# Performance work log

Hardware: AMD Instinct MI355X
Metric: run time of the kernel (lower is better)

Reference implementation:

```python
import jax, jax.numpy as jnp
import numpy as np
import math

D_MODEL = 64
D_STATE = 16
V_RANGE = 1
K = 3
BATCH, H, W = 4, 32, 32
V_LIST = [(x, y) for x in range(-V_RANGE, V_RANGE + 1) for y in range(-V_RANGE, V_RANGE + 1)]
NUM_V = len(V_LIST)


def _circ_conv(x, w):
    # x: (B, Cin, H, W), w: (Cout, Cin, K, K); circular padding then VALID conv
    p = K // 2
    xp = jnp.pad(x, ((0, 0), (0, 0), (p, p), (p, p)), mode='wrap')
    return jax.lax.conv_general_dilated(
        xp, w, window_strides=(1, 1), padding='VALID',
        dimension_numbers=('NCHW', 'OIHW', 'NCHW'))


def setup_inputs() -> dict:
    key = jax.random.key(0)
    ks = jax.random.split(key, 8)
    fan = 1.0 / math.sqrt(D_MODEL * K * K)
    u_t = jax.random.normal(ks[0], (BATCH, D_MODEL, H, W), dtype=jnp.float32)
    s_prev = jax.random.normal(ks[1], (BATCH, NUM_V, D_MODEL, D_STATE, H, W), dtype=jnp.float32)
    conv_delta_w = jax.random.normal(ks[2], (D_MODEL, D_MODEL, K, K), dtype=jnp.float32) * fan
    conv_delta_b = jax.random.normal(ks[3], (D_MODEL,), dtype=jnp.float32) * 0.01
    conv_B_w = jax.random.normal(ks[4], (D_STATE, D_MODEL, K, K), dtype=jnp.float32) * fan
    conv_C_w = jax.random.normal(ks[5], (D_STATE, D_MODEL, K, K), dtype=jnp.float32) * fan
    log_A_real = jnp.log(0.5 * jnp.ones((D_MODEL, D_STATE), dtype=jnp.float32))
    D = jnp.ones((D_MODEL,), dtype=jnp.float32)
    dt_inv_softplus = jnp.asarray(math.log(math.e - 1.0), dtype=jnp.float32)
    return {
        'u_t': u_t, 's_prev': s_prev,
        'conv_delta_w': conv_delta_w, 'conv_delta_b': conv_delta_b,
        'conv_B_w': conv_B_w, 'conv_C_w': conv_C_w,
        'log_A_real': log_A_real, 'D': D, 'dt_inv_softplus': dt_inv_softplus,
    }


def reference(u_t, s_prev, conv_delta_w, conv_delta_b, conv_B_w, conv_C_w,
              log_A_real, D, dt_inv_softplus):
    # delta: (B, d_model, h, w)
    delta = jax.nn.softplus(_circ_conv(u_t, conv_delta_w)
                            + conv_delta_b[None, :, None, None] + dt_inv_softplus)
    B_val = _circ_conv(u_t, conv_B_w)   # (B, d_state, h, w)
    C_val = _circ_conv(u_t, conv_C_w)   # (B, d_state, h, w)
    A = -jnp.exp(log_A_real)            # (d_model, d_state)
    A_bc = A[None, :, :, None, None]    # (1, d_model, d_state, 1, 1)
    A_bar = jnp.exp(delta[:, :, None] * A_bc)        # (B, d_model, d_state, h, w)
    B_bar = (A_bar - 1.0) / A_bc * B_val[:, None]    # (B, d_model, d_state, h, w)
    u_bc = u_t[:, :, None]              # (B, d_model, 1, h, w)
    C_bc = C_val[:, None]               # (B, 1, d_state, h, w)
    y_skip = u_t * D[None, :, None, None]

    s_next_list, y_list = [], []
    for i, (vx, vy) in enumerate(V_LIST):
        s_tr = jnp.roll(s_prev[:, i], shift=(-vy, -vx), axis=(-2, -1))
        s_new = A_bar * s_tr + B_bar * u_bc          # (B, d_model, d_state, h, w)
        y_new = jnp.sum(s_new * C_bc, axis=2) + y_skip
        s_next_list.append(s_new)
        y_list.append(y_new)
    s_next = jnp.stack(s_next_list, axis=1)  # (B, num_v, d_model, d_state, h, w)
    y_out = jnp.stack(y_list, axis=1)        # (B, num_v, d_model, h, w)
    return (y_out, s_next)
```

## Files before the change

### kernel.cpp

```cpp
#include <hip/hip_runtime.h>
#include <math.h>

#define NBATCH 4
#define NV 9
#define DM 64
#define DS 16

__global__ __launch_bounds__(256) void conv_kernel(
    const float* __restrict__ u, const float* __restrict__ wd,
    const float* __restrict__ bd, const float* __restrict__ wb,
    const float* __restrict__ wc, const float* __restrict__ dtp,
    float* __restrict__ delta_out, float* __restrict__ Bv_out,
    float* __restrict__ Cv_out)
{
    int bx = blockIdx.x;
    int ht = bx & 3;
    int co = (bx >> 2) % 96;
    int b  = bx / (4 * 96);
    int tid = threadIdx.x;
    int h = ht * 8 + (tid >> 5);
    int w = tid & 31;

    const float* wbase = (co < 64) ? (wd + (size_t)co * 576)
                       : (co < 80) ? (wb + (size_t)(co - 64) * 576)
                                   : (wc + (size_t)(co - 80) * 576);

    int wm = (w + 31) & 31, wp = (w + 1) & 31;
    int hm = (h + 31) & 31, hp = (h + 1) & 31;
    const float* ub = u + (size_t)b * 64 * 1024;

    float acc = 0.f;
    #pragma unroll 4
    for (int ci = 0; ci < 64; ++ci) {
        const float* up = ub + ci * 1024;
        const float* r0 = up + hm * 32;
        const float* r1 = up + h * 32;
        const float* r2 = up + hp * 32;
        const float* wq = wbase + ci * 9;
        acc += wq[0] * r0[wm] + wq[1] * r0[w] + wq[2] * r0[wp]
             + wq[3] * r1[wm] + wq[4] * r1[w] + wq[5] * r1[wp]
             + wq[6] * r2[wm] + wq[7] * r2[w] + wq[8] * r2[wp];
    }

    int pix = h * 32 + w;
    if (co < 64) {
        float x = acc + bd[co] + dtp[0];
        float d = (x > 20.f) ? x : log1pf(__expf(x));
        delta_out[((size_t)b * 64 + co) * 1024 + pix] = d;
    } else if (co < 80) {
        Bv_out[((size_t)b * 16 + (co - 64)) * 1024 + pix] = acc;
    } else {
        Cv_out[((size_t)b * 16 + (co - 80)) * 1024 + pix] = acc;
    }
}

__global__ __launch_bounds__(256) void scan_kernel(
    const float* __restrict__ u, const float* __restrict__ s_prev,
    const float* __restrict__ logA, const float* __restrict__ Dp,
    const float* __restrict__ delta_in, const float* __restrict__ Bv,
    const float* __restrict__ Cv,
    float* __restrict__ y_out, float* __restrict__ s_next)
{
    int bx = blockIdx.x;
    int t  = bx & 3;
    int c  = (bx >> 2) & 63;
    int bi = bx >> 8;
    int i  = bi % 9;
    int b  = bi / 9;

    int tid = threadIdx.x;
    int pix = t * 256 + tid;
    int h = pix >> 5, w = pix & 31;

    int vx = i / 3 - 1;
    int vy = i % 3 - 1;
    int hh = (h + vy + 32) & 31;
    int ww = (w + vx + 32) & 31;

    float uv = u[(((size_t)b * 64 + c) << 10) + pix];
    float dv = delta_in[(((size_t)b * 64 + c) << 10) + pix];
    float y  = uv * Dp[c];

    size_t chan = ((size_t)bi * 64 + c) * 16;
    const float* sp  = s_prev + (chan << 10) + hh * 32 + ww;
    float*       sn  = s_next + (chan << 10) + pix;
    const float* bvp = Bv + (((size_t)b * 16) << 10) + pix;
    const float* cvp = Cv + (((size_t)b * 16) << 10) + pix;
    const float* la  = logA + c * 16;

    #pragma unroll
    for (int n = 0; n < 16; ++n) {
        float A    = -__expf(la[n]);
        float ab   = __expf(dv * A);
        float coef = (ab - 1.0f) * __builtin_amdgcn_rcpf(A);
        float bu   = coef * bvp[(size_t)n << 10] * uv;
        float s    = sp[(size_t)n << 10];
        float v    = fmaf(ab, s, bu);
        sn[(size_t)n << 10] = v;
        y = fmaf(v, cvp[(size_t)n << 10], y);
    }
    y_out[((size_t)bi * 64 + c) * 1024 + pix] = y;
}

extern "C" void kernel_launch(void* const* d_in, const int* in_sizes, int n_in,
                              void* d_out, int out_size, void* d_ws, size_t ws_size,
                              hipStream_t stream) {
    const float* u      = (const float*)d_in[0];
    const float* s_prev = (const float*)d_in[1];
    const float* wd     = (const float*)d_in[2];
    const float* bd     = (const float*)d_in[3];
    const float* wb     = (const float*)d_in[4];
    const float* wc     = (const float*)d_in[5];
    const float* logA   = (const float*)d_in[6];
    const float* Dp     = (const float*)d_in[7];
    const float* dtp    = (const float*)d_in[8];

    float* ws    = (float*)d_ws;
    float* delta = ws;
    float* Bv    = ws + 262144;
    float* Cv    = ws + 327680;

    float* y_out  = (float*)d_out;
    float* s_next = y_out + (size_t)NBATCH * NV * DM * 1024;

    conv_kernel<<<dim3(4 * 96 * 4), dim3(256), 0, stream>>>(
        u, wd, bd, wb, wc, dtp, delta, Bv, Cv);
    scan_kernel<<<dim3(4 * 9 * 64 * 4), dim3(256), 0, stream>>>(
        u, s_prev, logA, Dp, delta, Bv, Cv, y_out, s_next);
}
```

Baseline: 120.8 us.

## Vectorize conv and scan kernels to four pixels per thread with float4

Both kernels now process four adjacent pixels per thread. The conv kernel uses float4 row loads plus halo scalars and float4 stores, with four accumulators that reuse loaded inputs across outputs. The scan kernel uses float4 loads and stores for state, B, C and y, and handles the horizontal roll with a lane shuffle inside groups of 8 lanes. Grid sizes shrink 4x, which lowers parallelism for the conv kernel (384 blocks) and raises per-thread register use.

```diff
diff --git a/kernel.cpp b/kernel.cpp
--- a/kernel.cpp
+++ b/kernel.cpp
@@ -5,6 +5,10 @@
 #define NV 9
 #define DM 64
 #define DS 16
+
+__device__ __forceinline__ float softplus_f(float x) {
+    return (x > 20.f) ? x : log1pf(__expf(x));
+}
 
 __global__ __launch_bounds__(256) void conv_kernel(
     const float* __restrict__ u, const float* __restrict__ wd,
@@ -14,43 +18,55 @@
     float* __restrict__ Cv_out)
 {
     int bx = blockIdx.x;
-    int ht = bx & 3;
-    int co = (bx >> 2) % 96;
-    int b  = bx / (4 * 96);
+    int co = bx % 96;
+    int b  = bx / 96;
     int tid = threadIdx.x;
-    int h = ht * 8 + (tid >> 5);
-    int w = tid & 31;
+    int row = tid >> 3;
+    int w0  = (tid & 7) << 2;
 
     const float* wbase = (co < 64) ? (wd + (size_t)co * 576)
                        : (co < 80) ? (wb + (size_t)(co - 64) * 576)
                                    : (wc + (size_t)(co - 80) * 576);
 
-    int wm = (w + 31) & 31, wp = (w + 1) & 31;
-    int hm = (h + 31) & 31, hp = (h + 1) & 31;
-    const float* ub = u + (size_t)b * 64 * 1024;
+    int hm = (row + 31) & 31, hp = (row + 1) & 31;
+    int wl = (w0 + 31) & 31;
+    int wr = (w0 + 4) & 31;
+    const float* ub = u + (size_t)b * 65536;
 
-    float acc = 0.f;
+    float a0 = 0.f, a1 = 0.f, a2 = 0.f, a3 = 0.f;
     #pragma unroll 4
     for (int ci = 0; ci < 64; ++ci) {
-        const float* up = ub + ci * 1024;
-        const float* r0 = up + hm * 32;
-        const float* r1 = up + h * 32;
-        const float* r2 = up + hp * 32;
+        const float* base = ub + ci * 1024;
         const float* wq = wbase + ci * 9;
-        acc += wq[0] * r0[wm] + wq[1] * r0[w] + wq[2] * r0[wp]
-             + wq[3] * r1[wm] + wq[4] * r1[w] + wq[5] * r1[wp]
-             + wq[6] * r2[wm] + wq[7] * r2[w] + wq[8] * r2[wp];
+        #pragma unroll
+        for (int r = 0; r < 3; ++r) {
+            int rr = (r == 0) ? hm : (r == 1) ? row : hp;
+            const float* rp = base + rr * 32;
+            float4 v = *(const float4*)(rp + w0);
+            float L = rp[wl], R = rp[wr];
+            float k0 = wq[r * 3 + 0], k1 = wq[r * 3 + 1], k2 = wq[r * 3 + 2];
+            a0 = fmaf(k0, L,   fmaf(k1, v.x, fmaf(k2, v.y, a0)));
+            a1 = fmaf(k0, v.x, fmaf(k1, v.y, fmaf(k2, v.z, a1)));
+            a2 = fmaf(k0, v.y, fmaf(k1, v.z, fmaf(k2, v.w, a2)));
+            a3 = fmaf(k0, v.z, fmaf(k1, v.w, fmaf(k2, R,   a3)));
+        }
     }
 
-    int pix = h * 32 + w;
+    int pix = row * 32 + w0;
     if (co < 64) {
-        float x = acc + bd[co] + dtp[0];
-        float d = (x > 20.f) ? x : log1pf(__expf(x));
-        delta_out[((size_t)b * 64 + co) * 1024 + pix] = d;
+        float bias = bd[co] + dtp[0];
+        float4 o;
+        o.x = softplus_f(a0 + bias);
+        o.y = softplus_f(a1 + bias);
+        o.z = softplus_f(a2 + bias);
+        o.w = softplus_f(a3 + bias);
+        *(float4*)(delta_out + (((size_t)b * 64 + co) << 10) + pix) = o;
     } else if (co < 80) {
-        Bv_out[((size_t)b * 16 + (co - 64)) * 1024 + pix] = acc;
+        *(float4*)(Bv_out + (((size_t)b * 16 + (co - 64)) << 10) + pix) =
+            make_float4(a0, a1, a2, a3);
     } else {
-        Cv_out[((size_t)b * 16 + (co - 80)) * 1024 + pix] = acc;
+        *(float4*)(Cv_out + (((size_t)b * 16 + (co - 80)) << 10) + pix) =
+            make_float4(a0, a1, a2, a3);
     }
 }
 
@@ -62,44 +78,81 @@
     float* __restrict__ y_out, float* __restrict__ s_next)
 {
     int bx = blockIdx.x;
-    int t  = bx & 3;
-    int c  = (bx >> 2) & 63;
-    int bi = bx >> 8;
-    int i  = bi % 9;
-    int b  = bi / 9;
+    int c  = bx & 63;
+    int bi9 = bx >> 6;
+    int i  = bi9 % 9;
+    int b  = bi9 / 9;
 
     int tid = threadIdx.x;
-    int pix = t * 256 + tid;
-    int h = pix >> 5, w = pix & 31;
-
+    int pix0 = tid << 2;
+    int h  = pix0 >> 5;
     int vx = i / 3 - 1;
     int vy = i % 3 - 1;
     int hh = (h + vy + 32) & 31;
-    int ww = (w + vx + 32) & 31;
 
-    float uv = u[(((size_t)b * 64 + c) << 10) + pix];
-    float dv = delta_in[(((size_t)b * 64 + c) << 10) + pix];
-    float y  = uv * Dp[c];
+    int lane = tid & 63;
+    int lnext = (lane & ~7) | ((lane + 1) & 7);
+    int lprev = (lane & ~7) | ((lane + 7) & 7);
 
-    size_t chan = ((size_t)bi * 64 + c) * 16;
-    const float* sp  = s_prev + (chan << 10) + hh * 32 + ww;
-    float*       sn  = s_next + (chan << 10) + pix;
-    const float* bvp = Bv + (((size_t)b * 16) << 10) + pix;
-    const float* cvp = Cv + (((size_t)b * 16) << 10) + pix;
+    size_t ubase = (((size_t)b * 64 + c) << 10) + pix0;
+    float4 u4 = *(const float4*)(u + ubase);
+    float4 d4 = *(const float4*)(delta_in + ubase);
+    float dk = Dp[c];
+    float4 y4 = make_float4(u4.x * dk, u4.y * dk, u4.z * dk, u4.w * dk);
+
+    size_t chan = ((size_t)bi9 * 64 + c) * 16;
+    const float* sp_row = s_prev + (chan << 10) + hh * 32;
+    float*       sn_px  = s_next + (chan << 10) + pix0;
+    const float* bvp = Bv + (((size_t)b * 16) << 10) + pix0;
+    const float* cvp = Cv + (((size_t)b * 16) << 10) + pix0;
     const float* la  = logA + c * 16;
+    int w0 = pix0 & 31;
 
-    #pragma unroll
+    #pragma unroll 4
     for (int n = 0; n < 16; ++n) {
-        float A    = -__expf(la[n]);
-        float ab   = __expf(dv * A);
-        float coef = (ab - 1.0f) * __builtin_amdgcn_rcpf(A);
-        float bu   = coef * bvp[(size_t)n << 10] * uv;
-        float s    = sp[(size_t)n << 10];
-        float v    = fmaf(ab, s, bu);
-        sn[(size_t)n << 10] = v;
-        y = fmaf(v, cvp[(size_t)n << 10], y);
+        float A  = -__expf(la[n]);
+        float rA = __builtin_amdgcn_rcpf(A);
+
+        float4 ab;
+        ab.x = __expf(d4.x * A);
+        ab.y = __expf(d4.y * A);
+        ab.z = __expf(d4.z * A);
+        ab.w = __expf(d4.w * A);
+
+        float4 b4 = *(const float4*)(bvp + ((size_t)n << 10));
+        float4 c4 = *(const float4*)(cvp + ((size_t)n << 10));
+
+        float4 bu;
+        bu.x = (ab.x - 1.f) * rA * b4.x * u4.x;
+        bu.y = (ab.y - 1.f) * rA * b4.y * u4.y;
+        bu.z = (ab.z - 1.f) * rA * b4.z * u4.z;
+        bu.w = (ab.w - 1.f) * rA * b4.w * u4.w;
+
+        float4 f = *(const float4*)(sp_row + ((size_t)n << 10) + w0);
+        float4 s4;
+        if (vx == 0) {
+            s4 = f;
+        } else if (vx > 0) {
+            float t = __shfl(f.x, lnext);
+            s4 = make_float4(f.y, f.z, f.w, t);
+        } else {
+            float t = __shfl(f.w, lprev);
+            s4 = make_float4(t, f.x, f.y, f.z);
+        }
+
+        float4 sn;
+        sn.x = fmaf(ab.x, s4.x, bu.x);
+        sn.y = fmaf(ab.y, s4.y, bu.y);
+        sn.z = fmaf(ab.z, s4.z, bu.z);
+        sn.w = fmaf(ab.w, s4.w, bu.w);
+        *(float4*)(sn_px + ((size_t)n << 10)) = sn;
+
+        y4.x = fmaf(sn.x, c4.x, y4.x);
+        y4.y = fmaf(sn.y, c4.y, y4.y);
+        y4.z = fmaf(sn.z, c4.z, y4.z);
+        y4.w = fmaf(sn.w, c4.w, y4.w);
     }
-    y_out[((size_t)bi * 64 + c) * 1024 + pix] = y;
+    *(float4*)(y_out + (((size_t)bi9 * 64 + c) << 10) + pix0) = y4;
 }
 
 extern "C" void kernel_launch(void* const* d_in, const int* in_sizes, int n_in,
@@ -123,8 +176,8 @@
     float* y_out  = (float*)d_out;
     float* s_next = y_out + (size_t)NBATCH * NV * DM * 1024;
 
-    conv_kernel<<<dim3(4 * 96 * 4), dim3(256), 0, stream>>>(
+    conv_kernel<<<dim3(4 * 96), dim3(256), 0, stream>>>(
         u, wd, bd, wb, wc, dtp, delta, Bv, Cv);
-    scan_kernel<<<dim3(4 * 9 * 64 * 4), dim3(256), 0, stream>>>(
+    scan_kernel<<<dim3(4 * 9 * 64), dim3(256), 0, stream>>>(
         u, s_prev, logA, Dp, delta, Bv, Cv, y_out, s_next);
 }
```

Result: slower. 154.4 us (+27.8%).
